# Optimization experiments

Measured on AMD Instinct MI355X. Metric: run time of the kernel, lower is better.

Reference implementation:

```python
import jax, jax.numpy as jnp
import numpy as np

B, C, W, H = 4, 256, 64, 64

def setup_inputs() -> dict:
    key = jax.random.key(0)
    ks = jax.random.split(key, 6)
    return {
        "fm_source": jax.random.normal(ks[0], (B, C, W, H), dtype=jnp.float32),
        "fm_reference": jax.random.normal(ks[1], (B, C, W, H), dtype=jnp.float32),
        "w_lambda": jax.random.normal(ks[2], (1, C, 1, 1), dtype=jnp.float32) * 0.05,
        "b_lambda": jax.random.normal(ks[3], (1,), dtype=jnp.float32) * 0.05,
        "w_beta": jax.random.normal(ks[4], (1, C, 1, 1), dtype=jnp.float32) * 0.05,
        "b_beta": jax.random.normal(ks[5], (1,), dtype=jnp.float32) * 0.05,
    }

def reference(fm_source, fm_reference, w_lambda, b_lambda, w_beta, b_beta):
    b, c, w, h = fm_reference.shape
    n = w * h
    # 1x1 convs on the reference feature map -> per-pixel scalars, flattened to [B, N]
    wl = w_lambda.reshape(c)
    wb = w_beta.reshape(c)
    ref_flat = fm_reference.reshape(b, c, n)   # [B, C, N]
    src_flat = fm_source.reshape(b, c, n)      # [B, C, N]
    old_lambda = jnp.einsum("bcn,c->bn", ref_flat, wl) + b_lambda[0]  # [B, N]
    old_beta = jnp.einsum("bcn,c->bn", ref_flat, wb) + b_beta[0]      # [B, N]
    # energy[b, i, j] = <src pixel i, ref pixel j> over channels
    energy = jnp.einsum("bci,bcj->bij", src_flat, ref_flat)  # [B, N, N]
    attention = jax.nn.softmax(energy, axis=-1)              # softmax over ref pixels j
    # new_lambda[b, i] = sum_j old_lambda[b, j] * attention[b, i, j]
    new_lambda = jnp.einsum("bj,bij->bi", old_lambda, attention).reshape(b, 1, w, h)
    new_beta = jnp.einsum("bj,bij->bi", old_beta, attention).reshape(b, 1, w, h)
    # broadcast modulation over the 256 channels
    return new_lambda * fm_source + new_beta
```

## Files before the change

### kernel.cpp

```cpp
#include <hip/hip_runtime.h>


#define B_ 4
#define C_ 256
#define N_ 4096
#define LOG2E 1.44269504f
#define SHIFT2 86.5617f
#define JSLICE 8
#define BN_ (B_ * N_)
#define NT_ 16

typedef _Float16 half_t;
typedef _Float16 v8h  __attribute__((ext_vector_type(8)));
typedef float    v16f __attribute__((ext_vector_type(16)));

#define GLDS16(g, l) __builtin_amdgcn_global_load_lds(                         \
    (const __attribute__((address_space(1))) void*)(g),                        \
    (__attribute__((address_space(3))) void*)(l), 16, 0, 0)

__global__ void k_prep(const float* __restrict__ src,
                       const float* __restrict__ ref,
                       const float* __restrict__ wl, const float* __restrict__ bl,
                       const float* __restrict__ wb, const float* __restrict__ bb,
                       half_t* __restrict__ s16, half_t* __restrict__ r16,
                       float* __restrict__ oldL, float* __restrict__ oldB) {
    if (blockIdx.z == 8) {
        int flat = blockIdx.y * 16 + blockIdx.x;
        int b  = flat & 3;
        int n0 = (flat >> 2) * 64;
        int nl = threadIdx.x & 63;
        int cq = threadIdx.x >> 6;
        const float* p = ref + ((size_t)b * C_ + cq * 64) * N_ + n0 + nl;
        float aL = 0.f, aB = 0.f;
#pragma unroll 8
        for (int c = 0; c < 64; c++) {
            float v = p[(size_t)c * N_];
            aL += v * wl[cq * 64 + c];
            aB += v * wb[cq * 64 + c];
        }
        __shared__ float red[8][64];
        red[cq][nl]     = aL;
        red[4 + cq][nl] = aB;
        __syncthreads();
        if (threadIdx.x < 64) {
            int t = threadIdx.x;
            oldL[(size_t)b * N_ + n0 + t] =
                red[0][t] + red[1][t] + red[2][t] + red[3][t] + bl[0];
        } else if (threadIdx.x < 128) {
            int t = threadIdx.x - 64;
            oldB[(size_t)b * N_ + n0 + t] =
                red[4][t] + red[5][t] + red[6][t] + red[7][t] + bb[0];
        }
        return;
    }
    __shared__ float tile[16][257];
    int z  = blockIdx.z;
    int b  = z & 3;
    const float* in  = (z < B_) ? src : ref;
    half_t*      out = (z < B_) ? s16 : r16;
    float scale      = (z < B_) ? LOG2E : 1.0f;
    int n0 = blockIdx.x * 256;
    int c0 = blockIdx.y * 16;
    int t    = threadIdx.x;
    int lane = t & 63;
    int wvid = t >> 6;
#pragma unroll
    for (int p = 0; p < 4; p++) {
        int c = p * 4 + wvid;
        float4 v = *(const float4*)(in + ((size_t)b * C_ + c0 + c) * N_ + n0 + lane * 4);
        tile[c][lane * 4 + 0] = v.x;
        tile[c][lane * 4 + 1] = v.y;
        tile[c][lane * 4 + 2] = v.z;
        tile[c][lane * 4 + 3] = v.w;
    }
    __syncthreads();
    int l31 = lane & 31, lhi = lane >> 5;
    size_t kb = (size_t)(c0 >> 4);
#pragma unroll
    for (int p = 0; p < 2; p++) {
        int tjl = p * 4 + wvid;
        v8h o;
#pragma unroll
        for (int e = 0; e < 8; e++)
            o[e] = (half_t)(tile[lhi * 8 + e][tjl * 32 + l31] * scale);
        size_t tj = (size_t)(n0 >> 5) + tjl;
        *(v8h*)(out + ((((size_t)b * 128 + tj) * 16 + kb) * 64 + lane) * 8) = o;
    }
}

__global__ __launch_bounds__(512, 2) void k_flash(
        const half_t* __restrict__ sT, const half_t* __restrict__ rT,
        const float* __restrict__ oldL, const float* __restrict__ oldB,
        float* __restrict__ part ) {
    __shared__ half_t lds[2][8192];
    int bid    = blockIdx.x;
    int b      = bid & 3;
    int jslice = (bid >> 2) & (JSLICE - 1);
    int iblock = bid >> 5;
    int tid    = threadIdx.x;
    int wv     = tid >> 6;
    int lane   = tid & 63;
    int l31    = lane & 31, lhi = lane >> 5;
    int ti     = iblock * 8 + wv;
    int i0     = ti * 32;
    int j0     = jslice * (N_ / JSLICE);
    int tj0    = j0 >> 5;

    const half_t* aP = sT + (((size_t)b * 128 + ti) * 16) * 512 + (size_t)lane * 8;
    v8h a[16];
#pragma unroll
    for (int kb = 0; kb < 16; kb++) a[kb] = *(const v8h*)(aP + (size_t)kb * 512);

    const half_t* bBase = rT + (((size_t)b * 128 + tj0) * 16) * 512;
    const float*  oLp = oldL + (size_t)b * N_ + j0 + l31;
    const float*  oBp = oldB + (size_t)b * N_ + j0 + l31;

    float sp[16], sl[16], sb[16];
#pragma unroll
    for (int r = 0; r < 16; r++) { sp[r] = 0.f; sl[r] = 0.f; sb[r] = 0.f; }

#pragma unroll
    for (int q = 0; q < 2; q++) {
        int chunk = q * 8 + wv;
        GLDS16(bBase + (size_t)chunk * 512 + (size_t)lane * 8,
               &lds[0][(size_t)chunk * 512]);
    }

    for (int jt = 0; jt < NT_; jt++) {
        __syncthreads();
        if (jt + 1 < NT_) {
            const half_t* g = bBase + (size_t)(jt + 1) * 8192;
#pragma unroll
            for (int q = 0; q < 2; q++) {
                int chunk = q * 8 + wv;
                GLDS16(g + (size_t)chunk * 512 + (size_t)lane * 8,
                       &lds[(jt + 1) & 1][(size_t)chunk * 512]);
            }
        }
        const half_t* bt = lds[jt & 1] + (size_t)lane * 8;
        v16f acc;
#pragma unroll
        for (int r = 0; r < 16; r++) acc[r] = -SHIFT2;
#pragma unroll
        for (int kb = 0; kb < 16; kb++) {
            v8h bf = *(const v8h*)(bt + (size_t)kb * 512);
            acc = __builtin_amdgcn_mfma_f32_32x32x16_f16(a[kb], bf, acc, 0, 0, 0);
        }
        float lam = oLp[jt * 32], bet = oBp[jt * 32];
#pragma unroll
        for (int r = 0; r < 16; r++) {
            float p = __builtin_amdgcn_exp2f(acc[r]);
            sp[r] += p;
            sl[r] += p * lam;
            sb[r] += p * bet;
        }
    }

    float* pSP = part + ((size_t)jslice * 3 + 0) * BN_;
    float* pSL = part + ((size_t)jslice * 3 + 1) * BN_;
    float* pSB = part + ((size_t)jslice * 3 + 2) * BN_;
#pragma unroll
    for (int r = 0; r < 16; r++) {
        float tp = sp[r], tl = sl[r], tb = sb[r];
#pragma unroll
        for (int m = 1; m <= 16; m <<= 1) {
            tp += __shfl_xor(tp, m, 64);
            tl += __shfl_xor(tl, m, 64);
            tb += __shfl_xor(tb, m, 64);
        }
        if (l31 == 0) {
            int row = (r & 3) + 8 * (r >> 2) + 4 * lhi;
            size_t ig = (size_t)b * N_ + i0 + row;
            pSP[ig] = tp; pSL[ig] = tl; pSB[ig] = tb;
        }
    }
}

__global__ void k_post(const float* __restrict__ src,
                       const float* __restrict__ part,
                       float* __restrict__ out) {
    int b  = blockIdx.x;
    int n0 = blockIdx.y * 1024;
    int c0 = blockIdx.z * 16;
    int t  = threadIdx.x;
    size_t bn = (size_t)b * N_ + n0 + t * 4;
    float4 sp = {0.f, 0.f, 0.f, 0.f}, sl = sp, sb = sp;
#pragma unroll
    for (int s = 0; s < JSLICE; s++) {
        float4 p0 = *(const float4*)(part + ((size_t)s * 3 + 0) * BN_ + bn);
        float4 p1 = *(const float4*)(part + ((size_t)s * 3 + 1) * BN_ + bn);
        float4 p2 = *(const float4*)(part + ((size_t)s * 3 + 2) * BN_ + bn);
        sp.x += p0.x; sp.y += p0.y; sp.z += p0.z; sp.w += p0.w;
        sl.x += p1.x; sl.y += p1.y; sl.z += p1.z; sl.w += p1.w;
        sb.x += p2.x; sb.y += p2.y; sb.z += p2.z; sb.w += p2.w;
    }
    float4 L, T;
    L.x = sl.x / sp.x; L.y = sl.y / sp.y; L.z = sl.z / sp.z; L.w = sl.w / sp.w;
    T.x = sb.x / sp.x; T.y = sb.y / sp.y; T.z = sb.z / sp.z; T.w = sb.w / sp.w;
    const float* sp0 = src + ((size_t)b * C_ + c0) * N_ + n0 + t * 4;
    float*       op0 = out + ((size_t)b * C_ + c0) * N_ + n0 + t * 4;
#pragma unroll 4
    for (int c = 0; c < 16; c++) {
        float4 v = *(const float4*)(sp0 + (size_t)c * N_);
        float4 o;
        o.x = L.x * v.x + T.x;
        o.y = L.y * v.y + T.y;
        o.z = L.z * v.z + T.z;
        o.w = L.w * v.w + T.w;
        *(float4*)(op0 + (size_t)c * N_) = o;
    }
}

extern "C" void kernel_launch(void* const* d_in, const int* in_sizes, int n_in,
                              void* d_out, int out_size, void* d_ws, size_t ws_size,
                              hipStream_t stream) {
    const float* src = (const float*)d_in[0];
    const float* ref = (const float*)d_in[1];
    const float* wl  = (const float*)d_in[2];
    const float* bl  = (const float*)d_in[3];
    const float* wb  = (const float*)d_in[4];
    const float* bb  = (const float*)d_in[5];
    float* out = (float*)d_out;

    float* oldL = (float*)d_ws;
    float* oldB = oldL + BN_;
    float* part = oldB + BN_;
    size_t needF  = ((size_t)2 + 3 * JSLICE) * BN_ * sizeof(float);
    size_t need16 = (size_t)2 * B_ * N_ * C_ * sizeof(half_t);
    half_t* s16;
    if (ws_size >= needF + need16) s16 = (half_t*)((char*)d_ws + needF);
    else                           s16 = (half_t*)d_out;
    half_t* r16 = s16 + (size_t)B_ * N_ * C_;

    k_prep<<<dim3(N_ / 256, C_ / 16, 9), 256, 0, stream>>>(
        src, ref, wl, bl, wb, bb, s16, r16, oldL, oldB);
    k_flash<<<512, 512, 0, stream>>>(s16, r16, oldL, oldB, part);
    k_post<<<dim3(B_, N_ / 1024, C_ / 16), 256, 0, stream>>>(src, part, out);
}
```

Baseline: 146.8 us.

## Retile prep transpose to 64x64 and split MFMA chain into two accumulators

The prep kernel now transposes 64x64 channel-by-pixel tiles instead of 16x256, which changes the grid shape and how the lane-to-output mapping is laid out. The oldL/oldB block indexing is adjusted to the new grid. In the flash kernel, the 16-step MFMA dependency chain is split into two independent accumulators of 8 steps each, summed before exp2. This is meant to hide MFMA latency, at the cost of 16 extra accumulator registers under the 512-thread, 2-block launch bounds.

```diff
diff --git a/kernel.cpp b/kernel.cpp
--- a/kernel.cpp
+++ b/kernel.cpp
@@ -12,6 +12,7 @@
 
 typedef _Float16 half_t;
 typedef _Float16 v8h  __attribute__((ext_vector_type(8)));
+typedef _Float16 v4h  __attribute__((ext_vector_type(4)));
 typedef float    v16f __attribute__((ext_vector_type(16)));
 
 #define GLDS16(g, l) __builtin_amdgcn_global_load_lds(                         \
@@ -25,9 +26,8 @@
                        half_t* __restrict__ s16, half_t* __restrict__ r16,
                        float* __restrict__ oldL, float* __restrict__ oldB) {
     if (blockIdx.z == 8) {
-        int flat = blockIdx.y * 16 + blockIdx.x;
-        int b  = flat & 3;
-        int n0 = (flat >> 2) * 64;
+        int b  = blockIdx.y;
+        int n0 = blockIdx.x * 64;
         int nl = threadIdx.x & 63;
         int cq = threadIdx.x >> 6;
         const float* p = ref + ((size_t)b * C_ + cq * 64) * N_ + n0 + nl;
@@ -53,38 +53,38 @@
         }
         return;
     }
-    __shared__ float tile[16][257];
+    __shared__ float tile[64][65];
     int z  = blockIdx.z;
     int b  = z & 3;
     const float* in  = (z < B_) ? src : ref;
     half_t*      out = (z < B_) ? s16 : r16;
     float scale      = (z < B_) ? LOG2E : 1.0f;
-    int n0 = blockIdx.x * 256;
-    int c0 = blockIdx.y * 16;
-    int t    = threadIdx.x;
-    int lane = t & 63;
-    int wvid = t >> 6;
-#pragma unroll
-    for (int p = 0; p < 4; p++) {
-        int c = p * 4 + wvid;
-        float4 v = *(const float4*)(in + ((size_t)b * C_ + c0 + c) * N_ + n0 + lane * 4);
-        tile[c][lane * 4 + 0] = v.x;
-        tile[c][lane * 4 + 1] = v.y;
-        tile[c][lane * 4 + 2] = v.z;
-        tile[c][lane * 4 + 3] = v.w;
+    int c0 = blockIdx.y * 64;
+    int n0 = blockIdx.x * 64;
+    int tx = threadIdx.x & 15, ty = threadIdx.x >> 4;
+#pragma unroll
+    for (int q = 0; q < 4; q++) {
+        int c = ty + q * 16;
+        float4 v = *(const float4*)(in + ((size_t)b * C_ + c0 + c) * N_ + n0 + tx * 4);
+        tile[c][tx * 4 + 0] = v.x;
+        tile[c][tx * 4 + 1] = v.y;
+        tile[c][tx * 4 + 2] = v.z;
+        tile[c][tx * 4 + 3] = v.w;
     }
     __syncthreads();
-    int l31 = lane & 31, lhi = lane >> 5;
-    size_t kb = (size_t)(c0 >> 4);
-#pragma unroll
-    for (int p = 0; p < 2; p++) {
-        int tjl = p * 4 + wvid;
+    int r   = threadIdx.x & 31;
+    int lhi = (threadIdx.x >> 5) & 1;
+    int wv  = threadIdx.x >> 6;
+#pragma unroll
+    for (int nt = 0; nt < 2; nt++) {
+        int nl = nt * 32 + r;
         v8h o;
 #pragma unroll
         for (int e = 0; e < 8; e++)
-            o[e] = (half_t)(tile[lhi * 8 + e][tjl * 32 + l31] * scale);
-        size_t tj = (size_t)(n0 >> 5) + tjl;
-        *(v8h*)(out + ((((size_t)b * 128 + tj) * 16 + kb) * 64 + lane) * 8) = o;
+            o[e] = (half_t)(tile[wv * 16 + lhi * 8 + e][nl] * scale);
+        size_t tj = (size_t)(n0 >> 5) + nt;
+        size_t kb = (size_t)(c0 >> 4) + wv;
+        *(v8h*)(out + ((((size_t)b * 128 + tj) * 16 + kb) * 64 + (threadIdx.x & 63)) * 8) = o;
     }
 }
 
@@ -138,18 +138,20 @@
             }
         }
         const half_t* bt = lds[jt & 1] + (size_t)lane * 8;
-        v16f acc;
-#pragma unroll
-        for (int r = 0; r < 16; r++) acc[r] = -SHIFT2;
-#pragma unroll
-        for (int kb = 0; kb < 16; kb++) {
-            v8h bf = *(const v8h*)(bt + (size_t)kb * 512);
-            acc = __builtin_amdgcn_mfma_f32_32x32x16_f16(a[kb], bf, acc, 0, 0, 0);
+        v16f acc0, acc1;
+#pragma unroll
+        for (int r = 0; r < 16; r++) { acc0[r] = -SHIFT2; acc1[r] = 0.f; }
+#pragma unroll
+        for (int kb = 0; kb < 8; kb++) {
+            acc0 = __builtin_amdgcn_mfma_f32_32x32x16_f16(
+                a[kb],     *(const v8h*)(bt + (size_t)kb * 512),       acc0, 0, 0, 0);
+            acc1 = __builtin_amdgcn_mfma_f32_32x32x16_f16(
+                a[kb + 8], *(const v8h*)(bt + (size_t)(kb + 8) * 512), acc1, 0, 0, 0);
         }
         float lam = oLp[jt * 32], bet = oBp[jt * 32];
 #pragma unroll
         for (int r = 0; r < 16; r++) {
-            float p = __builtin_amdgcn_exp2f(acc[r]);
+            float p = __builtin_amdgcn_exp2f(acc0[r] + acc1[r]);
             sp[r] += p;
             sl[r] += p * lam;
             sb[r] += p * bet;
@@ -232,7 +234,7 @@
     else                           s16 = (half_t*)d_out;
     half_t* r16 = s16 + (size_t)B_ * N_ * C_;
 
-    k_prep<<<dim3(N_ / 256, C_ / 16, 9), 256, 0, stream>>>(
+    k_prep<<<dim3(N_ / 64, C_ / 64, 9), 256, 0, stream>>>(
         src, ref, wl, bl, wb, bb, s16, r16, oldL, oldB);
     k_flash<<<512, 512, 0, stream>>>(s16, r16, oldL, oldB, part);
     k_post<<<dim3(B_, N_ / 1024, C_ / 16), 256, 0, stream>>>(src, part, out);
```

Result: faster. 143.2 us (-2.4%).
